# Kernel optimization log

Hardware: AMD Instinct MI355X
Metric: run time of the kernel (lower is better)

The kernel has to match this reference:

```python
import jax, jax.numpy as jnp
import numpy as np

DN = ('NCHW', 'OIHW', 'NCHW')


def conv2d(x, w, b):
    y = jax.lax.conv_general_dilated(x, w, (1, 1), 'SAME', dimension_numbers=DN)
    return y + b[None, :, None, None]


def dyn_filter(x, Wa, ba, Wb, bb, Wc, bc):
    # KPN-style head: predict 81 per-pixel 9x9 filter taps, softmax-normalized.
    h = jax.nn.relu(conv2d(x, Wa, ba))
    h = jax.nn.relu(conv2d(h, Wb, bb))
    f = conv2d(h, Wc, bc)            # (N, 81, H, W)
    return jax.nn.softmax(f, axis=1)


def apply_dynamic_conv(x, f):
    # Equivalent to pad(4) + unfold(9x9) + mul + sum, without materializing
    # the (N,81,H,W)*... patch tensor: accumulate 81 shifted slices.
    N, C, H, W = x.shape  # C == 1
    xp = jnp.pad(x, ((0, 0), (0, 0), (4, 4), (4, 4)))
    out = jnp.zeros((N, 1, H, W), x.dtype)
    for dy in range(9):
        for dx in range(9):
            k = dy * 9 + dx  # matches unfold(2).unfold(3).permute(0,1,4,5,2,3) tap order
            out = out + xp[:, :, dy:dy + H, dx:dx + W] * f[:, k:k + 1]
    return out


def nearest_resize(x, oh, ow):
    _, _, ih, iw = x.shape
    ri = jnp.arange(oh) * ih // oh   # matches torch F.interpolate mode='nearest'
    rj = jnp.arange(ow) * iw // ow
    return x[:, :, ri][:, :, :, rj]


def setup_inputs() -> dict:
    key = jax.random.key(0)
    ks = jax.random.split(key, 8)
    s = 0.05
    return {
        'x': jax.random.normal(ks[0], (2, 1, 512, 512), jnp.float32),
        'g': jax.random.normal(ks[1], (2, 1, 512, 512), jnp.float32),
        'fWa': jax.random.normal(ks[2], (5, 64, 1, 3, 3), jnp.float32) * s,
        'fba': jnp.zeros((5, 64), jnp.float32),
        'fWb': jax.random.normal(ks[3], (5, 64, 64, 3, 3), jnp.float32) * s,
        'fbb': jnp.zeros((5, 64), jnp.float32),
        'fWc': jax.random.normal(ks[4], (5, 81, 64, 3, 3), jnp.float32) * s,
        'fbc': jnp.zeros((5, 81), jnp.float32),
        'W2a': jax.random.normal(ks[5], (64, 5, 3, 3), jnp.float32) * s,
        'b2a': jnp.zeros((64,), jnp.float32),
        'W2b': jax.random.normal(ks[6], (1, 64, 3, 3), jnp.float32) * s,
        'b2b': jnp.zeros((1,), jnp.float32),
    }


def reference(x, g, fWa, fba, fWb, fbb, fWc, fbc, W2a, b2a, W2b, b2b):
    N, C, h, w = x.shape
    scales = [
        x,
        nearest_resize(x, h // 2, w // 2),
        nearest_resize(x, h // 4, w // 4),
        nearest_resize(x, h // 8, w // 8),
        g,
    ]
    outs = []
    for i, s in enumerate(scales):
        f = dyn_filter(s, fWa[i], fba[i], fWb[i], fbb[i], fWc[i], fbc[i])
        y = apply_dynamic_conv(s, f)
        if y.shape[2] != h or y.shape[3] != w:
            y = nearest_resize(y, h, w)
        outs.append(y)
    cat = jnp.concatenate(outs, axis=1)  # (N, 5, h, w)
    hid = jax.nn.relu(conv2d(cat, W2a, b2a))
    return conv2d(hid, W2b, b2b)
```

## Files before the change

### kernel.cpp

```cpp
#include <hip/hip_runtime.h>
#include <math.h>

typedef _Float16 half8 __attribute__((ext_vector_type(8)));
typedef _Float16 half4v __attribute__((ext_vector_type(4)));
typedef float f32x4 __attribute__((ext_vector_type(4)));

#define LOG2E 1.44269504f

__device__ __forceinline__ void pack_generic(int rem, int NT, int COUT, float scale,
                                             const float* __restrict__ src,
                                             _Float16* __restrict__ dst) {
  int j = rem & 7, lane = (rem >> 3) & 63, rest = rem >> 9;
  int t = rest % NT, s = rest / NT;
  int oc = t * 16 + (lane & 15);
  int tap = s >> 1;
  int ic = (s & 1) * 32 + ((lane >> 4) & 3) * 8 + j;
  float v = (oc < COUT) ? src[((size_t)oc * 64 + ic) * 9 + tap] * scale : 0.f;
  dst[rem] = (_Float16)v;
}

__global__ void prep_all_kernel(const float* __restrict__ fWa, const float* __restrict__ fWb,
                                const float* __restrict__ fWc, const float* __restrict__ W2a,
                                const float* __restrict__ W2b, const float* __restrict__ x,
                                _Float16* __restrict__ Bp1, _Float16* __restrict__ BpA,
                                _Float16* __restrict__ BpB, _Float16* __restrict__ Bpb,
                                _Float16* __restrict__ Bpc,
                                _Float16* __restrict__ s1, _Float16* __restrict__ s2,
                                _Float16* __restrict__ s3) {
  int idx = blockIdx.x * blockDim.x + threadIdx.x;
  if (idx < 184320) {
    int sc = idx / 36864, rem = idx - sc * 36864;
    pack_generic(rem, 4, 64, 1.f, fWb + sc * 36864, Bpb + sc * 36864);
  } else if (idx < 460800) {
    int i2 = idx - 184320;
    int sc = i2 / 55296, rem = i2 - sc * 55296;
    pack_generic(rem, 6, 81, LOG2E, fWc + sc * 46656, Bpc + sc * 55296);
  } else if (idx < 471040) {
    int i2 = idx - 460800;
    int sc = i2 >> 11, rem = i2 & 2047;
    int j = rem & 7, lane = (rem >> 3) & 63, nt = rem >> 9;
    int oc = nt * 16 + (lane & 15);
    int k = ((lane >> 4) & 3) * 8 + j;
    float v = (k < 9) ? fWa[sc * 576 + oc * 9 + k] : 0.f;
    Bp1[sc * 2048 + rem] = (_Float16)v;
  } else if (idx < 475136) {
    int rem = idx - 471040;
    int j = rem & 7, lane = (rem >> 3) & 63;
    int nt = (rem >> 9) & 3, s = rem >> 11;
    int oc = nt * 16 + (lane & 15);
    int k = s * 32 + ((lane >> 4) & 3) * 8 + j;
    float v = 0.f;
    if (k < 45) { int ic = k / 9, tap = k - ic * 9; v = W2a[(oc * 5 + ic) * 9 + tap]; }
    BpA[rem] = (_Float16)v;
  } else if (idx < 484352) {
    pack_generic(idx - 475136, 1, 1, 1.f, W2b, BpB);
  } else if (idx < 615424) {
    int i2 = idx - 484352;
    int n = i2 >> 16, p = i2 & 65535, rr = p >> 8, cc = p & 255;
    s1[i2] = (_Float16)x[(size_t)n * 262144 + (size_t)(rr * 2) * 512 + cc * 2];
  } else if (idx < 648192) {
    int i2 = idx - 615424;
    int n = i2 >> 14, p = i2 & 16383, rr = p >> 7, cc = p & 127;
    s2[i2] = (_Float16)x[(size_t)n * 262144 + (size_t)(rr * 4) * 512 + cc * 4];
  } else if (idx < 656384) {
    int i2 = idx - 648192;
    int n = i2 >> 12, p = i2 & 4095, rr = p >> 6, cc = p & 63;
    s3[i2] = (_Float16)x[(size_t)n * 262144 + (size_t)(rr * 8) * 512 + cc * 8];
  }
}

__device__ __forceinline__ int xcd_swizzle(int bid) {
  return (bid & 7) * 596 + (bid >> 3);
}

__device__ __forceinline__ void map_block(int bid, int& sc, int& n, int& bx, int& by,
                                          int& Hs, int& RS, int& h2off) {
  if (bid < 2048) { sc = 0; Hs = 512; RS = 1; h2off = 0;
    int t = bid; n = t >> 10; t &= 1023; by = t >> 5; bx = t & 31; }
  else if (bid < 4096) { sc = 4; Hs = 512; RS = 1; h2off = 33554432;
    int t = bid - 2048; n = t >> 10; t &= 1023; by = t >> 5; bx = t & 31; }
  else if (bid < 4608) { sc = 1; Hs = 256; RS = 2; h2off = 67108864;
    int t = bid - 4096; n = t >> 8; t &= 255; by = t >> 4; bx = t & 15; }
  else if (bid < 4736) { sc = 2; Hs = 128; RS = 4; h2off = 75497472;
    int t = bid - 4608; n = t >> 6; t &= 63; by = t >> 3; bx = t & 7; }
  else { sc = 3; Hs = 64; RS = 8; h2off = 77594624;
    int t = bid - 4736; n = t >> 4; t &= 15; by = t >> 2; bx = t & 3; }
}

__device__ __forceinline__ const void* pick_src(int sc, const float* x, const float* g,
                                                const _Float16* s1, const _Float16* s2,
                                                const _Float16* s3, int& sStr, bool& f16s) {
  if (sc == 0) { sStr = 262144; f16s = false; return x; }
  if (sc == 1) { sStr = 65536; f16s = true; return s1; }
  if (sc == 2) { sStr = 16384; f16s = true; return s2; }
  if (sc == 3) { sStr = 4096; f16s = true; return s3; }
  sStr = 262144; f16s = false; return g;
}

__device__ __forceinline__ float src_load(const void* p, bool f16s, size_t off) {
  return f16s ? (float)((const _Float16*)p)[off] : ((const float*)p)[off];
}

template <int MT, int NT, bool SWAP>
__device__ __forceinline__ void mfma_acc18(const _Float16* slab, const half8* __restrict__ Bp,
                                           f32x4 (&acc)[MT][NT], int tid) {
  const int lane = tid & 63;
  const int wv = tid >> 6;
  const int quad = lane >> 4;
  const int ln15 = lane & 15;
  const f32x4 zz = {0.f, 0.f, 0.f, 0.f};
#pragma unroll
  for (int mt = 0; mt < MT; ++mt)
#pragma unroll
    for (int nt = 0; nt < NT; ++nt) acc[mt][nt] = zz;
  auto step = [&](int s, half8 (&bf)[NT]) {
    const int tap = s >> 1;
    const int dy = tap / 3;
    const int dx = tap - dy * 3;
    const int C = dx + ln15;
    const int qsw = (((s & 1) * 4 + quad) ^ (C & 7));
    const _Float16* base = slab + C * 64 + qsw * 8;
    half8 af[MT];
#pragma unroll
    for (int mt = 0; mt < MT; ++mt)
      af[mt] = *(const half8*)(base + (wv * MT + mt + dy) * (18 * 64));
#pragma unroll
    for (int mt = 0; mt < MT; ++mt)
#pragma unroll
      for (int nt = 0; nt < NT; ++nt)
        acc[mt][nt] = SWAP
          ? __builtin_amdgcn_mfma_f32_16x16x32_f16(bf[nt], af[mt], acc[mt][nt], 0, 0, 0)
          : __builtin_amdgcn_mfma_f32_16x16x32_f16(af[mt], bf[nt], acc[mt][nt], 0, 0, 0);
  };
  half8 bA[NT], bB[NT];
#pragma unroll
  for (int nt = 0; nt < NT; ++nt) bA[nt] = Bp[nt * 64 + lane];
#pragma unroll 1
  for (int i = 0; i < 9; ++i) {
    const int s0 = 2 * i, s1 = 2 * i + 1;
    const int s2 = (s1 + 1 < 18) ? s1 + 1 : 17;
#pragma unroll
    for (int nt = 0; nt < NT; ++nt) bB[nt] = Bp[(s1 * NT + nt) * 64 + lane];
    step(s0, bA);
#pragma unroll
    for (int nt = 0; nt < NT; ++nt) bA[nt] = Bp[(s2 * NT + nt) * 64 + lane];
    step(s1, bB);
  }
}

template <int MT, int NT, int COUT, int COUTP, bool RELU, typename OutT>
__device__ __forceinline__ void mfma_body(const _Float16* slab, const half8* __restrict__ Bp,
                                          const float* __restrict__ bias,
                                          OutT* __restrict__ out,
                                          int H, int W, int gr0, int gc0, int tid) {
  f32x4 acc[MT][NT];
  mfma_acc18<MT, NT, false>(slab, Bp, acc, tid);
  const int lane = tid & 63;
  const int wv = tid >> 6;
  const int quad = lane >> 4;
  const int ln15 = lane & 15;
  float bvv[NT];
#pragma unroll
  for (int nt = 0; nt < NT; ++nt) {
    const int oc = nt * 16 + ln15;
    bvv[nt] = (oc < COUT) ? bias[oc] : 0.f;
  }
#pragma unroll
  for (int mt = 0; mt < MT; ++mt) {
    const int gr = gr0 + wv * MT + mt;
#pragma unroll
    for (int reg = 0; reg < 4; ++reg) {
      const int gc = gc0 + quad * 4 + reg;
#pragma unroll
      for (int nt = 0; nt < NT; ++nt) {
        const int oc = nt * 16 + ln15;
        float v = acc[mt][nt][reg] + bvv[nt];
        if (RELU) v = fmaxf(v, 0.f);
        if (oc < COUTP) out[((size_t)gr * W + gc) * COUTP + oc] = (OutT)v;
      }
    }
  }
}

__global__ __launch_bounds__(512, 4)
void conv12_ms_kernel(const float* __restrict__ x, const float* __restrict__ g,
                      const _Float16* __restrict__ s1, const _Float16* __restrict__ s2,
                      const _Float16* __restrict__ s3,
                      const half8* __restrict__ Bp1b, const float* __restrict__ fba,
                      const half8* __restrict__ Bpbb, const float* __restrict__ fbb,
                      _Float16* __restrict__ h2) {
  __shared__ float xs[20 * 20];
  __shared__ __align__(16) _Float16 slab[18 * 18 * 64];
  int sc, n, bx, by, Hs, RS, h2off;
  map_block(xcd_swizzle(blockIdx.x), sc, n, bx, by, Hs, RS, h2off);
  int sStr; bool f16s;
  const void* src = pick_src(sc, x, g, s1, s2, s3, sStr, f16s);
  _Float16* out = h2 + h2off + (size_t)n * Hs * Hs * 64;
  const half8* Bp1 = Bp1b + sc * 256;
  const half8* Bp = Bpbb + sc * 4608;
  const float* ba = fba + sc * 64;
  const float* bb = fbb + sc * 64;
  const int H = Hs, W = Hs;
  const int tid = threadIdx.x;
  const int gr0 = by * 16, gc0 = bx * 16;
  for (int i = tid; i < 400; i += 512) {
    int R = i / 20, C = i % 20;
    int gr = gr0 - 2 + R, gc = gc0 - 2 + C;
    xs[i] = (gr >= 0 && gr < H && gc >= 0 && gc < W)
                ? src_load(src, f16s, (size_t)n * sStr + (size_t)gr * W + gc) : 0.f;
  }
  __syncthreads();
  const int lane = tid & 63;
  const int wv = tid >> 6;
  const int quad = lane >> 4;
  const int ln15 = lane & 15;
  half8 bf1[4];
  float b1v[4][4];
#pragma unroll
  for (int nt = 0; nt < 4; ++nt) {
    bf1[nt] = Bp1[nt * 64 + lane];
#pragma unroll
    for (int reg = 0; reg < 4; ++reg) b1v[nt][reg] = ba[nt * 16 + quad * 4 + reg];
  }
  int off1[8];
  bool v1[8];
#pragma unroll
  for (int j = 0; j < 8; ++j) {
    int k = quad * 8 + j;
    v1[j] = (k < 9);
    off1[j] = v1[j] ? ((k / 3) * 20 + (k % 3)) : 0;
  }
  const f32x4 zz = {0.f, 0.f, 0.f, 0.f};
#pragma unroll 1
  for (int mt = wv; mt < 21; mt += 8) {
    int p = mt * 16 + ln15;
    int pcl = (p < 323) ? p : 323;
    int Rg = pcl / 18, Cg = pcl - Rg * 18;
    int base = Rg * 20 + Cg;
    half8 af;
#pragma unroll
    for (int j = 0; j < 8; ++j)
      af[j] = v1[j] ? (_Float16)xs[base + off1[j]] : (_Float16)0.f;
    f32x4 a1[4] = {zz, zz, zz, zz};
#pragma unroll
    for (int nt = 0; nt < 4; ++nt)
      a1[nt] = __builtin_amdgcn_mfma_f32_16x16x32_f16(bf1[nt], af, a1[nt], 0, 0, 0);
    if (p < 324) {
      int R2 = p / 18, C2 = p - R2 * 18;
      int gr = gr0 - 1 + R2, gc = gc0 - 1 + C2;
      bool inb = (gr >= 0 && gr < H && gc >= 0 && gc < W);
      _Float16* sb = slab + p * 64 + (quad & 1) * 4;
      const int csw = C2 & 7;
#pragma unroll
      for (int nt = 0; nt < 4; ++nt) {
        half4v w;
#pragma unroll
        for (int reg = 0; reg < 4; ++reg) {
          float v = inb ? fmaxf(a1[nt][reg] + b1v[nt][reg], 0.f) : 0.f;
          w[reg] = (_Float16)v;
        }
        const int chunk = nt * 2 + (quad >> 1);
        *(half4v*)(sb + ((chunk ^ csw) * 8)) = w;
      }
    }
  }
  __syncthreads();
  mfma_body<2, 4, 64, 64, true, _Float16>(slab, Bp, bb, out, H, W, gr0, gc0, tid);
}

__global__ __launch_bounds__(512, 4)
void conv3sd_ms_kernel(const _Float16* __restrict__ h2, const half8* __restrict__ Bpcb,
                       const float* __restrict__ fbc,
                       const float* __restrict__ x, const float* __restrict__ g,
                       const _Float16* __restrict__ s1, const _Float16* __restrict__ s2,
                       const _Float16* __restrict__ s3, float* __restrict__ cat) {
  constexpr int MT = 2;
  __shared__ __align__(16) _Float16 slab[324 * 40];
  __shared__ float xs[24 * 24];
  int sc, n, bx, by, Hs, RS, h2off;
  map_block(xcd_swizzle(blockIdx.x), sc, n, bx, by, Hs, RS, h2off);
  int sStr; bool f16s;
  const void* src = pick_src(sc, x, g, s1, s2, s3, sStr, f16s);
  const _Float16* in = h2 + h2off + (size_t)n * Hs * Hs * 64;
  const half8* Bp = Bpcb + sc * 6912;
  const float* bias = fbc + sc * 81;
  float* catp = cat + (size_t)(sc * 2 + n) * 262144;
  const int H = Hs, W = Hs;
  const int tid = threadIdx.x;
  const int gr0 = by * 16, gc0 = bx * 16;
  const int lane = tid & 63;
  const int wv = tid >> 6;
  const int quad = lane >> 4;
  const int ln15 = lane & 15;
  for (int i = tid; i < 576; i += 512) {
    int R = i / 24, C = i % 24;
    int gr = gr0 - 4 + R, gc = gc0 - 4 + C;
    xs[i] = (gr >= 0 && gr < H && gc >= 0 && gc < W)
                ? src_load(src, f16s, (size_t)n * sStr + (size_t)gr * W + gc) : 0.f;
  }
  auto stage_load = [&](int h, half8 (&stg)[3], int (&soff)[3], bool (&sok)[3]) {
#pragma unroll
    for (int it = 0; it < 3; ++it) {
      int i = tid + it * 512;
      bool ok = (i < 1296);
      int chunk = i & 3, px = i >> 2;
      int R = px / 18, C = px - R * 18;
      int gr = gr0 - 1 + R, gc = gc0 - 1 + C;
      half8 v = {0, 0, 0, 0, 0, 0, 0, 0};
      if (ok && gr >= 0 && gr < H && gc >= 0 && gc < W)
        v = *(const half8*)(in + ((size_t)gr * W + gc) * 64 + (h * 4 + chunk) * 8);
      stg[it] = v;
      soff[it] = px * 40 + chunk * 8;
      sok[it] = ok;
    }
  };
  auto stage_write = [&](half8 (&stg)[3], int (&soff)[3], bool (&sok)[3]) {
#pragma unroll
    for (int it = 0; it < 3; ++it)
      if (sok[it]) *(half8*)(slab + soff[it]) = stg[it];
  };

  f32x4 acc[MT][6];
  const f32x4 zz = {0.f, 0.f, 0.f, 0.f};
#pragma unroll
  for (int mt = 0; mt < MT; ++mt)
#pragma unroll
    for (int nt = 0; nt < 6; ++nt) acc[mt][nt] = zz;

  auto ctap = [&](int tap, half8 (&bf)[6]) {
    const int dy = tap / 3;
    const int dx = tap - dy * 3;
    const int C = dx + ln15;
    const _Float16* base = slab + C * 40 + quad * 8;
    half8 af[MT];
#pragma unroll
    for (int mt = 0; mt < MT; ++mt)
      af[mt] = *(const half8*)(base + (wv * MT + mt + dy) * 720);
#pragma unroll
    for (int mt = 0; mt < MT; ++mt)
#pragma unroll
      for (int nt = 0; nt < 6; ++nt)
        acc[mt][nt] = __builtin_amdgcn_mfma_f32_16x16x32_f16(bf[nt], af[mt], acc[mt][nt], 0, 0, 0);
  };
  auto run_taps = [&](int h) {
    half8 bA[6], bB[6];
#pragma unroll
    for (int nt = 0; nt < 6; ++nt) bA[nt] = Bp[(h * 6 + nt) * 64 + lane];
#pragma unroll 1
    for (int i = 0; i < 4; ++i) {
      const int t1 = 2 * i + 1, t2 = 2 * i + 2;
#pragma unroll
      for (int nt = 0; nt < 6; ++nt) bB[nt] = Bp[(((t1 * 2 + h) * 6) + nt) * 64 + lane];
      ctap(2 * i, bA);
#pragma unroll
      for (int nt = 0; nt < 6; ++nt) bA[nt] = Bp[(((t2 * 2 + h) * 6) + nt) * 64 + lane];
      ctap(t1, bB);
    }
    ctap(8, bA);
  };

  half8 stgA[3]; int soffA[3]; bool sokA[3];
  half8 stgB[3]; int soffB[3]; bool sokB[3];
  stage_load(0, stgA, soffA, sokA);
  stage_write(stgA, soffA, sokA);
  __syncthreads();
  stage_load(1, stgB, soffB, sokB);
  run_taps(0);
  __syncthreads();
  stage_write(stgB, soffB, sokB);
  __syncthreads();
  run_taps(1);

  float bvv[6][4];
  int dyx[6][4];
  bool vv[6][4];
#pragma unroll
  for (int nt = 0; nt < 6; ++nt)
#pragma unroll
    for (int reg = 0; reg < 4; ++reg) {
      int ch = nt * 16 + quad * 4 + reg;
      bool ok = (ch < 81);
      vv[nt][reg] = ok;
      bvv[nt][reg] = ok ? bias[ch] * LOG2E : 0.f;
      int dy = ch / 9, dx = ch - dy * 9;
      dyx[nt][reg] = ok ? dy * 24 + dx : 0;
    }
  const int lrs = (RS == 2) ? 1 : ((RS == 4) ? 2 : 3);
#pragma unroll
  for (int mt = 0; mt < MT; ++mt) {
    const float* xb = xs + (wv * MT + mt) * 24 + ln15;
    float sum = 0.f, y = 0.f;
#pragma unroll
    for (int nt = 0; nt < 6; ++nt)
#pragma unroll
      for (int reg = 0; reg < 4; ++reg) {
        if (vv[nt][reg]) {
          float e = exp2f(acc[mt][nt][reg] + bvv[nt][reg]);
          sum += e;
          y = fmaf(e, xb[dyx[nt][reg]], y);
        }
      }
    sum += __shfl_xor(sum, 16, 64);
    sum += __shfl_xor(sum, 32, 64);
    y += __shfl_xor(y, 16, 64);
    y += __shfl_xor(y, 32, 64);
    const float o = y / sum;
    const int gr = gr0 + wv * MT + mt, gc = gc0 + ln15;
    if (RS == 1) {
      if (quad == 0) catp[(size_t)gr * 512 + gc] = o;
    } else {
      for (int t = quad; t < RS * RS; t += 4) {
        int a = t >> lrs, b = t & (RS - 1);
        catp[((size_t)(gr * RS + a)) * 512 + (gc * RS + b)] = o;
      }
    }
  }
}

__global__ __launch_bounds__(512, 4)
void tail_fused_kernel(const float* __restrict__ cat,
                       const half8* __restrict__ BpA, const float* __restrict__ b2a,
                       const half8* __restrict__ BpB, const float* __restrict__ b2b,
                       float* __restrict__ out) {
  __shared__ float cs[20 * 20 * 5];
  __shared__ __align__(16) _Float16 hid[18 * 18 * 64];
  const int n = blockIdx.z;
  float* op = out + (size_t)n * (512 * 512);
  const int tid = threadIdx.x;
  const int gr0 = blockIdx.y * 16, gc0 = blockIdx.x * 16;
  for (int i = tid; i < 2000; i += 512) {
    int ic = i / 400, px = i - ic * 400;
    int R = px / 20, C = px - R * 20;
    int gr = gr0 - 2 + R, gc = gc0 - 2 + C;
    cs[px * 5 + ic] = (gr >= 0 && gr < 512 && gc >= 0 && gc < 512)
                ? cat[(size_t)(ic * 2 + n) * 262144 + (size_t)gr * 512 + gc] : 0.f;
  }
  __syncthreads();
  const int lane = tid & 63;
  const int wv = tid >> 6;
  const int quad = lane >> 4;
  const int ln15 = lane & 15;
  int goff[2][8];
  bool gok[2][8];
#pragma unroll
  for (int s = 0; s < 2; ++s)
#pragma unroll
    for (int j = 0; j < 8; ++j) {
      int k = s * 32 + quad * 8 + j;
      bool ok = (k < 45);
      int ic = k / 9;
      int tap = k - ic * 9;
      int dy = tap / 3, dx = tap - dy * 3;
      goff[s][j] = ok ? ((dy * 20 + dx) * 5 + ic) : 0;
      gok[s][j] = ok;
    }
  half8 bfA[2][4];
  float bAv[4][4];
#pragma unroll
  for (int s = 0; s < 2; ++s)
#pragma unroll
    for (int nt = 0; nt < 4; ++nt) bfA[s][nt] = BpA[(s * 4 + nt) * 64 + lane];
#pragma unroll
  for (int nt = 0; nt < 4; ++nt)
#pragma unroll
    for (int reg = 0; reg < 4; ++reg) bAv[nt][reg] = b2a[nt * 16 + quad * 4 + reg];
  const f32x4 zz = {0.f, 0.f, 0.f, 0.f};
#pragma unroll 1
  for (int mt = wv; mt < 21; mt += 8) {
    int p = mt * 16 + ln15;
    int pcl = (p < 323) ? p : 323;
    int base = (pcl / 18) * 100 + (pcl % 18) * 5;
    f32x4 acc1[4] = {zz, zz, zz, zz};
#pragma unroll
    for (int s = 0; s < 2; ++s) {
      half8 af;
#pragma unroll
      for (int j = 0; j < 8; ++j) {
        float a = gok[s][j] ? cs[base + goff[s][j]] : 0.f;
        af[j] = (_Float16)a;
      }
#pragma unroll
      for (int nt = 0; nt < 4; ++nt)
        acc1[nt] = __builtin_amdgcn_mfma_f32_16x16x32_f16(bfA[s][nt], af, acc1[nt], 0, 0, 0);
    }
    if (p < 324) {
      int R2 = p / 18, C2 = p - R2 * 18;
      int gr = gr0 - 1 + R2, gc = gc0 - 1 + C2;
      bool inb = (gr >= 0 && gr < 512 && gc >= 0 && gc < 512);
      _Float16* sb = hid + p * 64 + (quad & 1) * 4;
      const int csw = C2 & 7;
#pragma unroll
      for (int nt = 0; nt < 4; ++nt) {
        half4v w;
#pragma unroll
        for (int reg = 0; reg < 4; ++reg) {
          float v = inb ? fmaxf(acc1[nt][reg] + bAv[nt][reg], 0.f) : 0.f;
          w[reg] = (_Float16)v;
        }
        const int chunk = nt * 2 + (quad >> 1);
        *(half4v*)(sb + ((chunk ^ csw) * 8)) = w;
      }
    }
  }
  __syncthreads();
  mfma_body<2, 1, 1, 1, false, float>(hid, BpB, b2b, op, 512, 512, gr0, gc0, tid);
}

extern "C" void kernel_launch(void* const* d_in, const int* in_sizes, int n_in,
                              void* d_out, int out_size, void* d_ws, size_t ws_size,
                              hipStream_t stream) {
  (void)in_sizes; (void)n_in; (void)out_size; (void)ws_size;
  const float* x   = (const float*)d_in[0];
  const float* g   = (const float*)d_in[1];
  const float* fWa = (const float*)d_in[2];
  const float* fba = (const float*)d_in[3];
  const float* fWb = (const float*)d_in[4];
  const float* fbb = (const float*)d_in[5];
  const float* fWc = (const float*)d_in[6];
  const float* fbc = (const float*)d_in[7];
  const float* W2a = (const float*)d_in[8];
  const float* b2a = (const float*)d_in[9];
  const float* W2b = (const float*)d_in[10];
  const float* b2b = (const float*)d_in[11];
  float* out = (float*)d_out;
  float* ws = (float*)d_ws;

  float* Bp1F = ws;
  float* BpAF = Bp1F + 5120;
  float* BpBF = BpAF + 2048;
  float* BpbF = BpBF + 4608;
  float* BpcF = BpbF + 92160;
  float* s1F  = BpcF + 138240;
  float* s2F  = s1F + 65536;
  float* s3F  = s2F + 16384;
  float* cat  = s3F + 4096;
  float* h2F  = cat + 2621440;
  _Float16* s1 = (_Float16*)s1F;
  _Float16* s2 = (_Float16*)s2F;
  _Float16* s3 = (_Float16*)s3F;
  _Float16* h2 = (_Float16*)h2F;
  const half8* Bp1 = (const half8*)Bp1F;
  const half8* BpA = (const half8*)BpAF;
  const half8* BpB = (const half8*)BpBF;
  const half8* Bpb = (const half8*)BpbF;
  const half8* Bpc = (const half8*)BpcF;

  prep_all_kernel<<<2564, 256, 0, stream>>>(fWa, fWb, fWc, W2a, W2b, x,
                                            (_Float16*)Bp1F, (_Float16*)BpAF,
                                            (_Float16*)BpBF, (_Float16*)BpbF,
                                            (_Float16*)BpcF, s1, s2, s3);
  conv12_ms_kernel<<<4768, 512, 0, stream>>>(x, g, s1, s2, s3, Bp1, fba, Bpb, fbb, h2);
  conv3sd_ms_kernel<<<4768, 512, 0, stream>>>(h2, Bpc, fbc, x, g, s1, s2, s3, cat);
  tail_fused_kernel<<<dim3(32, 32, 2), 512, 0, stream>>>(cat, BpA, b2a, BpB, b2b, out);
}
```

Before: 393.0 us.

## Stage MFMA weight fragments through double-buffered shared memory

Replaces per-wave direct global loads of packed B (weight) fragments with cooperative, double-buffered staging into LDS, two taps per chunk, across the conv12, conv3 and tail kernels. Each block now fetches each weight slice once instead of every wave reloading it from global/L2. In exchange it adds a __syncthreads per chunk, extra LDS footprint that may reduce occupancy, and LDS read traffic competing with the activation slab reads.

```diff
diff --git a/kernel.cpp b/kernel.cpp
--- a/kernel.cpp
+++ b/kernel.cpp
@@ -101,8 +101,9 @@
   return f16s ? (float)((const _Float16*)p)[off] : ((const float*)p)[off];
 }
 
-template <int MT, int NT, bool SWAP>
+template <int MT, int NT, bool SWAP, int NTHR>
 __device__ __forceinline__ void mfma_acc18(const _Float16* slab, const half8* __restrict__ Bp,
+                                           half8* __restrict__ Bs,
                                            f32x4 (&acc)[MT][NT], int tid) {
   const int lane = tid & 63;
   const int wv = tid >> 6;
@@ -132,29 +133,36 @@
           ? __builtin_amdgcn_mfma_f32_16x16x32_f16(bf[nt], af[mt], acc[mt][nt], 0, 0, 0)
           : __builtin_amdgcn_mfma_f32_16x16x32_f16(af[mt], bf[nt], acc[mt][nt], 0, 0, 0);
   };
-  half8 bA[NT], bB[NT];
-#pragma unroll
-  for (int nt = 0; nt < NT; ++nt) bA[nt] = Bp[nt * 64 + lane];
+  constexpr int CH = 2 * NT * 64;
+  for (int i = tid; i < CH; i += NTHR) Bs[i] = Bp[i];
+  __syncthreads();
 #pragma unroll 1
-  for (int i = 0; i < 9; ++i) {
-    const int s0 = 2 * i, s1 = 2 * i + 1;
-    const int s2 = (s1 + 1 < 18) ? s1 + 1 : 17;
-#pragma unroll
-    for (int nt = 0; nt < NT; ++nt) bB[nt] = Bp[(s1 * NT + nt) * 64 + lane];
-    step(s0, bA);
-#pragma unroll
-    for (int nt = 0; nt < NT; ++nt) bA[nt] = Bp[(s2 * NT + nt) * 64 + lane];
-    step(s1, bB);
-  }
-}
-
-template <int MT, int NT, int COUT, int COUTP, bool RELU, typename OutT>
+  for (int c = 0; c < 9; ++c) {
+    const int buf = c & 1;
+    if (c < 8) {
+      const half8* gsrc = Bp + (2 * (c + 1)) * (NT * 64);
+      half8* dst = Bs + (buf ^ 1) * CH;
+      for (int i = tid; i < CH; i += NTHR) dst[i] = gsrc[i];
+    }
+    half8 bf[NT];
+#pragma unroll
+    for (int nt = 0; nt < NT; ++nt) bf[nt] = Bs[buf * CH + nt * 64 + lane];
+    step(2 * c, bf);
+#pragma unroll
+    for (int nt = 0; nt < NT; ++nt) bf[nt] = Bs[buf * CH + NT * 64 + nt * 64 + lane];
+    step(2 * c + 1, bf);
+    __syncthreads();
+  }
+}
+
+template <int MT, int NT, int COUT, int COUTP, bool RELU, typename OutT, int NTHR>
 __device__ __forceinline__ void mfma_body(const _Float16* slab, const half8* __restrict__ Bp,
+                                          half8* __restrict__ Bs,
                                           const float* __restrict__ bias,
                                           OutT* __restrict__ out,
                                           int H, int W, int gr0, int gc0, int tid) {
   f32x4 acc[MT][NT];
-  mfma_acc18<MT, NT, false>(slab, Bp, acc, tid);
+  mfma_acc18<MT, NT, false, NTHR>(slab, Bp, Bs, acc, tid);
   const int lane = tid & 63;
   const int wv = tid >> 6;
   const int quad = lane >> 4;
@@ -191,6 +199,7 @@
                       _Float16* __restrict__ h2) {
   __shared__ float xs[20 * 20];
   __shared__ __align__(16) _Float16 slab[18 * 18 * 64];
+  __shared__ half8 BsS[2 * 2 * 4 * 64];
   int sc, n, bx, by, Hs, RS, h2off;
   map_block(xcd_swizzle(blockIdx.x), sc, n, bx, by, Hs, RS, h2off);
   int sStr; bool f16s;
@@ -265,7 +274,7 @@
     }
   }
   __syncthreads();
-  mfma_body<2, 4, 64, 64, true, _Float16>(slab, Bp, bb, out, H, W, gr0, gc0, tid);
+  mfma_body<2, 4, 64, 64, true, _Float16, 512>(slab, Bp, BsS, bb, out, H, W, gr0, gc0, tid);
 }
 
 __global__ __launch_bounds__(512, 4)
@@ -277,6 +286,7 @@
   constexpr int MT = 2;
   __shared__ __align__(16) _Float16 slab[324 * 40];
   __shared__ float xs[24 * 24];
+  __shared__ half8 BsS[2 * 768];
   int sc, n, bx, by, Hs, RS, h2off;
   map_block(xcd_swizzle(blockIdx.x), sc, n, bx, by, Hs, RS, h2off);
   int sStr; bool f16s;
@@ -319,6 +329,21 @@
     for (int it = 0; it < 3; ++it)
       if (sok[it]) *(half8*)(slab + soff[it]) = stg[it];
   };
+  auto stageB2 = [&](int t0, int t1, int h, int buf) {
+    half8* dst = BsS + buf * 768;
+    const half8* g0 = Bp + (size_t)(t0 * 2 + h) * 384;
+    const half8* g1 = Bp + (size_t)(t1 * 2 + h) * 384;
+#pragma unroll
+    for (int it = 0; it < 2; ++it) {
+      int i = tid + it * 512;
+      if (i < 768) dst[i] = (i < 384) ? g0[i] : g1[i - 384];
+    }
+  };
+  auto stageB1 = [&](int h, int buf) {
+    half8* dst = BsS + buf * 768;
+    const half8* g0 = Bp + (size_t)(16 + h) * 384;
+    if (tid < 384) dst[tid] = g0[tid];
+  };
 
   f32x4 acc[MT][6];
   const f32x4 zz = {0.f, 0.f, 0.f, 0.f};
@@ -342,34 +367,41 @@
       for (int nt = 0; nt < 6; ++nt)
         acc[mt][nt] = __builtin_amdgcn_mfma_f32_16x16x32_f16(bf[nt], af[mt], acc[mt][nt], 0, 0, 0);
   };
-  auto run_taps = [&](int h) {
-    half8 bA[6], bB[6];
-#pragma unroll
-    for (int nt = 0; nt < 6; ++nt) bA[nt] = Bp[(h * 6 + nt) * 64 + lane];
+  auto run_taps = [&](int h, int b0) {
 #pragma unroll 1
-    for (int i = 0; i < 4; ++i) {
-      const int t1 = 2 * i + 1, t2 = 2 * i + 2;
-#pragma unroll
-      for (int nt = 0; nt < 6; ++nt) bB[nt] = Bp[(((t1 * 2 + h) * 6) + nt) * 64 + lane];
-      ctap(2 * i, bA);
-#pragma unroll
-      for (int nt = 0; nt < 6; ++nt) bA[nt] = Bp[(((t2 * 2 + h) * 6) + nt) * 64 + lane];
-      ctap(t1, bB);
-    }
-    ctap(8, bA);
+    for (int c = 0; c < 4; ++c) {
+      const int buf = b0 ^ (c & 1);
+      if (c < 3) stageB2(2 * c + 2, 2 * c + 3, h, buf ^ 1);
+      else       stageB1(h, buf ^ 1);
+      half8 bf[6];
+#pragma unroll
+      for (int nt = 0; nt < 6; ++nt) bf[nt] = BsS[buf * 768 + nt * 64 + lane];
+      ctap(2 * c, bf);
+#pragma unroll
+      for (int nt = 0; nt < 6; ++nt) bf[nt] = BsS[buf * 768 + 384 + nt * 64 + lane];
+      ctap(2 * c + 1, bf);
+      __syncthreads();
+    }
+    const int buf = b0;
+    half8 bf[6];
+#pragma unroll
+    for (int nt = 0; nt < 6; ++nt) bf[nt] = BsS[buf * 768 + nt * 64 + lane];
+    ctap(8, bf);
   };
 
   half8 stgA[3]; int soffA[3]; bool sokA[3];
   half8 stgB[3]; int soffB[3]; bool sokB[3];
   stage_load(0, stgA, soffA, sokA);
   stage_write(stgA, soffA, sokA);
+  stageB2(0, 1, 0, 0);
   __syncthreads();
   stage_load(1, stgB, soffB, sokB);
-  run_taps(0);
+  run_taps(0, 0);
   __syncthreads();
   stage_write(stgB, soffB, sokB);
-  __syncthreads();
-  run_taps(1);
+  stageB2(0, 1, 1, 0);
+  __syncthreads();
+  run_taps(1, 0);
 
   float bvv[6][4];
   int dyx[6][4];
@@ -424,6 +456,7 @@
                        float* __restrict__ out) {
   __shared__ float cs[20 * 20 * 5];
   __shared__ __align__(16) _Float16 hid[18 * 18 * 64];
+  __shared__ half8 BsS[2 * 2 * 1 * 64];
   const int n = blockIdx.z;
   float* op = out + (size_t)n * (512 * 512);
   const int tid = threadIdx.x;
@@ -503,7 +536,7 @@
     }
   }
   __syncthreads();
-  mfma_body<2, 1, 1, 1, false, float>(hid, BpB, b2b, op, 512, 512, gr0, gc0, tid);
+  mfma_body<2, 1, 1, 1, false, float, 512>(hid, BpB, BsS, b2b, op, 512, 512, gr0, gc0, tid);
 }
 
 extern "C" void kernel_launch(void* const* d_in, const int* in_sizes, int n_in,
```

Result: faster. 377.4 us (-4.0%).
